# Kernel tuning notes

Measured on AMD Instinct MI355X. Metric: run time of the kernel, lower is better.

## Reference

```python
import jax, jax.numpy as jnp
import numpy as np

N, E, H, F, T = 50000, 800000, 64, 74, 4
STEPS = 4


def setup_inputs() -> dict:
    key = jax.random.key(0)
    ks = jax.random.split(key, 16)
    s = 0.05
    return {
        "x": jax.random.normal(ks[0], (N, F), jnp.float32),
        "etype": jax.random.randint(ks[1], (E,), 0, T, jnp.int32),
        "src": jax.random.randint(ks[2], (E,), 0, N, jnp.int32),
        "dst": jax.random.randint(ks[3], (E,), 0, N, jnp.int32),
        "W_in": jax.random.normal(ks[4], (F, H), jnp.float32) * s,
        "b_in": jax.random.normal(ks[5], (H,), jnp.float32) * s,
        "edge_W": jax.random.normal(ks[6], (T, H, H), jnp.float32) * s,
        "edge_b": jax.random.normal(ks[7], (T, 1), jnp.float32) * s,
        "gru_Wih": jax.random.normal(ks[8], (H, 3 * H), jnp.float32) * s,
        "gru_Whh": jax.random.normal(ks[9], (H, 3 * H), jnp.float32) * s,
        "gru_bih": jax.random.normal(ks[10], (3 * H,), jnp.float32) * s,
        "gru_bhh": jax.random.normal(ks[11], (3 * H,), jnp.float32) * s,
        "mlp_W1": jax.random.normal(ks[12], (2 * H, H), jnp.float32) * s,
        "mlp_b1": jax.random.normal(ks[13], (H,), jnp.float32) * s,
        "mlp_W2": jax.random.normal(ks[14], (H, H), jnp.float32) * s,
        "mlp_b2": jax.random.normal(ks[15], (H,), jnp.float32) * s,
    }


def _gru_cell(x, h, Wih, Whh, bih, bhh):
    gi = x @ Wih + bih  # [N, 3H]
    gh = h @ Whh + bhh
    ir, iz, inn = jnp.split(gi, 3, axis=-1)
    hr, hz, hn = jnp.split(gh, 3, axis=-1)
    r = jax.nn.sigmoid(ir + hr)
    z = jax.nn.sigmoid(iz + hz)
    n = jnp.tanh(inn + r * hn)
    return (1.0 - z) * n + z * h


def reference(x, etype, src, dst, W_in, b_in, edge_W, edge_b,
              gru_Wih, gru_Whh, gru_bih, gru_bhh,
              mlp_W1, mlp_b1, mlp_W2, mlp_b2):
    h_init = x @ W_in + b_in  # [N, H]
    h = h_init
    for _ in range(STEPS):
        # per-node transform under every edge type: [N, T, H]
        nt = jnp.einsum('ni,tio->nto', h, edge_W)
        # gather per-edge message from src node + per-type bias, ReLU
        msg = jax.nn.relu(nt[src, etype] + edge_b[etype])  # [E, H]
        agg = jax.ops.segment_sum(msg, dst, num_segments=N)  # [N, H]
        h = _gru_cell(agg, h, gru_Wih, gru_Whh, gru_bih, gru_bhh)
    cat = jnp.concatenate([h_init, h], axis=-1)  # [N, 2H]
    out = jnp.tanh(jax.nn.relu(cat @ mlp_W1 + mlp_b1) @ mlp_W2 + mlp_b2)
    return out
```

## Files before the change

kernel.cpp:

```cpp
#include <hip/hip_runtime.h>
#include <hip/hip_bf16.h>

#define N_NODES 50000
#define M2      50048
#define N_EDGES 800000
#define H 64
#define F 74
#define T 4
#define STEPS 4
#define NTILES16 (M2/16)
#define PAD_REC  (M2*4)
#define SCAN_NB  196

using short8 = __attribute__((ext_vector_type(8))) short;
using f32x4  = __attribute__((ext_vector_type(4))) float;
typedef unsigned short ushort_t;

#define MFMA(a,b,c) __builtin_amdgcn_mfma_f32_16x16x32_bf16(a,b,c,0,0,0)

static __device__ inline float b2f(ushort_t u) {
    union { unsigned int i; float f; } c; c.i = ((unsigned int)u) << 16; return c.f;
}
static __device__ inline ushort_t f2b(float v) {
    union { __hip_bfloat16 b; ushort_t u; } c; c.b = __float2bfloat16(v); return c.u;
}
static __device__ inline void split_store(ushort_t* hi, ushort_t* lo, size_t ix, float v) {
    ushort_t h = f2b(v);
    hi[ix] = h;
    lo[ix] = f2b(v - b2f(h));
}
static __device__ inline float sigm(float x) { return 1.f / (1.f + __expf(-x)); }
static __device__ inline float tanh_f(float x) {
    float e2 = __expf(2.f * x); return 1.f - 2.f / (e2 + 1.f);
}

template<int KW8>
static __device__ inline void stage_tile(const ushort_t* __restrict__ g, ushort_t* l,
                                         int rows, int tid, int nthr) {
    const int chunks = rows * KW8;
    for (int i = tid; i < chunks; i += nthr) {
        int row = i / KW8, kg = i - row * KW8;
        short8 v = *(const short8*)(g + (size_t)row * (KW8 * 8) + kg * 8);
        int b = (row * (KW8 * 16) + kg * 16) ^ ((row & 7) << 4);
        *(short8*)((char*)l + b) = v;
    }
}
template<int KW8>
static __device__ inline short8 rdfrag(const ushort_t* l, int row, int kg) {
    int b = (row * (KW8 * 16) + kg * 16) ^ ((row & 7) << 4);
    return *(const short8*)((const char*)l + b);
}
static __device__ inline short8 afrag(const ushort_t* base, int LD, int row, int kg) {
    return *(const short8*)(base + (size_t)row * LD + kg * 8);
}

__global__ __launch_bounds__(256) void prep_w_kernel(
    const float* __restrict__ W_in, const float* __restrict__ eW,
    const float* __restrict__ Wih, const float* __restrict__ Whh,
    const float* __restrict__ W1, const float* __restrict__ W2,
    const float* __restrict__ x,
    ushort_t* __restrict__ BtWin_hi, ushort_t* __restrict__ BtWin_lo,
    ushort_t* __restrict__ BtE_hi,
    ushort_t* __restrict__ BtgHi, ushort_t* __restrict__ BtgLo,
    ushort_t* __restrict__ BtW1_hi, ushort_t* __restrict__ BtW1_lo,
    ushort_t* __restrict__ BtW2_hi, ushort_t* __restrict__ BtW2_lo,
    int* __restrict__ deg, ushort_t* __restrict__ ntr_pad,
    ushort_t* __restrict__ x_hi, ushort_t* __restrict__ x_lo)
{
    int idx = blockIdx.x * 256 + threadIdx.x;
    if (idx < 6144) {
        int col = idx / 96, k = idx - col * 96;
        float v = (k < F) ? W_in[(size_t)k * 64 + col] : 0.f;
        split_store(BtWin_hi, BtWin_lo, idx, v);
    } else if (idx < 22528) {
        int i = idx - 6144;
        int c = i >> 6, k = i & 63;
        float v = eW[(c >> 6) * 4096 + k * 64 + (c & 63)];
        BtE_hi[i] = f2b(v);
    } else if (idx < 47104) {
        int i = idx - 22528;
        int hh = i / 12288;
        int r2 = i - hh * 12288;
        int rr = r2 >> 7, k = r2 & 127;
        int gg = rr >> 5, cc = rr & 31;
        int col = gg * 64 + hh * 32 + cc;
        float v = (k < 64) ? Wih[(size_t)k * 192 + col]
                           : Whh[(size_t)(k - 64) * 192 + col];
        BtgHi[i] = f2b(v);
    } else if (idx < 55296) {
        int i = idx - 47104;
        int hh = i >> 12;
        int r2 = i & 4095;
        int cc = r2 >> 7, k = r2 & 127;
        int col = 128 + hh * 32 + cc;
        float v = (k < 64) ? Wih[(size_t)k * 192 + col]
                           : Whh[(size_t)(k - 64) * 192 + col];
        ushort_t h = f2b(v);
        BtgLo[i] = f2b(v - b2f(h));
    } else if (idx < 63488) {
        int i = idx - 55296;
        int col = i >> 7, k = i & 127;
        float v = W1[(size_t)k * 64 + col];
        split_store(BtW1_hi, BtW1_lo, i, v);
    } else if (idx < 67584) {
        int i = idx - 63488;
        int col = i >> 6, k = i & 63;
        float v = W2[(size_t)k * 64 + col];
        split_store(BtW2_hi, BtW2_lo, i, v);
    } else if (idx < 117584) {
        deg[idx - 67584] = 0;
    } else if (idx < 117648) {
        ntr_pad[idx - 117584] = 0;
    } else {
        int i = idx - 117648;
        if (i < M2 * 96) {
            int row = i / 96, c = i - row * 96;
            float v = (row < N_NODES && c < F) ? x[(size_t)row * F + c] : 0.f;
            split_store(x_hi, x_lo, i, v);
        }
    }
}

__global__ __launch_bounds__(256) void degrank_kernel(
    const int* __restrict__ dst, int* __restrict__ deg, int* __restrict__ rank)
{
    int e = blockIdx.x * 256 + threadIdx.x;
    if (e < N_EDGES) rank[e] = atomicAdd(&deg[dst[e]], 1);
}

__global__ __launch_bounds__(256) void scan_p1(
    const int* __restrict__ deg, int* __restrict__ bsum)
{
    __shared__ int ws4[4];
    const int tid = threadIdx.x, lane = tid & 63, w = tid >> 6;
    int idx = blockIdx.x * 256 + tid;
    int v = (idx < N_NODES) ? deg[idx] : 0;
#pragma unroll
    for (int off = 32; off >= 1; off >>= 1) v += __shfl_down(v, off, 64);
    if (lane == 0) ws4[w] = v;
    __syncthreads();
    if (tid == 0) bsum[blockIdx.x] = ws4[0] + ws4[1] + ws4[2] + ws4[3];
}

__global__ __launch_bounds__(256) void scan_p2(
    const int* __restrict__ bsum, int* __restrict__ boff, int* __restrict__ rowp)
{
    __shared__ int ws4[4];
    const int tid = threadIdx.x, lane = tid & 63, w = tid >> 6;
    int v = (tid < SCAN_NB) ? bsum[tid] : 0;
    int x = v;
#pragma unroll
    for (int off = 1; off < 64; off <<= 1) {
        int u = __shfl_up(x, off, 64);
        if (lane >= off) x += u;
    }
    if (lane == 63) ws4[w] = x;
    __syncthreads();
    int a0 = ws4[0], a1 = ws4[1], a2 = ws4[2];
    int add = (w > 0 ? a0 : 0) + (w > 1 ? a1 : 0) + (w > 2 ? a2 : 0);
    if (tid < SCAN_NB) boff[tid] = add + x - v;
    if (tid == 255) rowp[N_NODES] = add + x;
}

__global__ __launch_bounds__(256) void scan_p3(
    const int* __restrict__ deg, const int* __restrict__ boff,
    int* __restrict__ rowp)
{
    __shared__ int ws4[4];
    const int tid = threadIdx.x, lane = tid & 63, w = tid >> 6;
    int idx = blockIdx.x * 256 + tid;
    int v = (idx < N_NODES) ? deg[idx] : 0;
    int x = v;
#pragma unroll
    for (int off = 1; off < 64; off <<= 1) {
        int u = __shfl_up(x, off, 64);
        if (lane >= off) x += u;
    }
    if (lane == 63) ws4[w] = x;
    __syncthreads();
    int a0 = ws4[0], a1 = ws4[1], a2 = ws4[2];
    int add = boff[blockIdx.x]
            + (w > 0 ? a0 : 0) + (w > 1 ? a1 : 0) + (w > 2 ? a2 : 0);
    if (idx < N_NODES) rowp[idx] = add + x - v;
}

__global__ __launch_bounds__(256) void fill2_kernel(
    const int* __restrict__ src, const int* __restrict__ etype,
    const int* __restrict__ dst, const int* __restrict__ rowp,
    const int* __restrict__ rank, int* __restrict__ ss)
{
    int e = blockIdx.x * 256 + threadIdx.x;
    if (e < N_EDGES)
        ss[rowp[dst[e]] + rank[e]] = src[e] * 4 + etype[e];
}

__global__ __launch_bounds__(256) void init_gemm(
    const ushort_t* __restrict__ xhi, const ushort_t* __restrict__ xlo,
    const ushort_t* __restrict__ Bh, const ushort_t* __restrict__ Bl,
    const float* __restrict__ b_in,
    ushort_t* __restrict__ h_hi, ushort_t* __restrict__ h_lo,
    ushort_t* __restrict__ hin_hi, ushort_t* __restrict__ hin_lo)
{
    __shared__ ushort_t lds[12288];
    ushort_t* LBh = lds;
    ushort_t* LBl = lds + 6144;
    const int tid = threadIdx.x, lane = tid & 63, wid = tid >> 6;
    const int lr = lane & 15, g = lane >> 4;
    stage_tile<12>(Bh, LBh, 64, tid, 256);
    stage_tile<12>(Bl, LBl, 64, tid, 256);
    __syncthreads();
    for (int wt = blockIdx.x * 4 + wid; wt < NTILES16; wt += gridDim.x * 4) {
        const ushort_t* pAh = xhi + (size_t)wt * 16 * 96;
        const ushort_t* pAl = xlo + (size_t)wt * 16 * 96;
        f32x4 acc[4];
        f32x4 zz = {0.f, 0.f, 0.f, 0.f};
#pragma unroll
        for (int f = 0; f < 4; ++f) acc[f] = zz;
#pragma unroll
        for (int ks = 0; ks < 3; ++ks) {
            int kg = ks * 4 + g;
            short8 ah = afrag(pAh, 96, lr, kg);
            short8 al = afrag(pAl, 96, lr, kg);
#pragma unroll
            for (int f = 0; f < 4; ++f) {
                short8 bh = rdfrag<12>(LBh, f * 16 + lr, kg);
                short8 bl = rdfrag<12>(LBl, f * 16 + lr, kg);
                acc[f] = MFMA(ah, bh, acc[f]);
                acc[f] = MFMA(ah, bl, acc[f]);
                acc[f] = MFMA(al, bh, acc[f]);
            }
        }
#pragma unroll
        for (int f = 0; f < 4; ++f) {
            int o = lr + f * 16;
            float b = b_in[o];
#pragma unroll
            for (int q = 0; q < 4; ++q) {
                int m = wt * 16 + g * 4 + q;
                if (m < N_NODES) {
                    float v = acc[f][q] + b;
                    split_store(h_hi, h_lo, (size_t)m * 64 + o, v);
                    split_store(hin_hi, hin_lo, (size_t)m * 64 + o, v);
                }
            }
        }
    }
}

__global__ __launch_bounds__(512, 2) void nt_gemm(
    const ushort_t* __restrict__ hhi,
    const ushort_t* __restrict__ Bh,
    const float* __restrict__ edge_b, ushort_t* __restrict__ ntr)
{
    __shared__ ushort_t lds[16384];
    const int tid = threadIdx.x, lane = tid & 63, wid = tid >> 6;
    const int lr = lane & 15, g = lane >> 4;
    stage_tile<8>(Bh, lds, 256, tid, 512);
    __syncthreads();
    for (int wt = blockIdx.x * 8 + wid; wt < NTILES16; wt += gridDim.x * 8) {
        const ushort_t* pA = hhi + (size_t)wt * 16 * 64;
        f32x4 acc[16];
        f32x4 zz = {0.f, 0.f, 0.f, 0.f};
#pragma unroll
        for (int f = 0; f < 16; ++f) acc[f] = zz;
#pragma unroll
        for (int ks = 0; ks < 2; ++ks) {
            int kg = ks * 4 + g;
            short8 ah = afrag(pA, 64, lr, kg);
#pragma unroll
            for (int f = 0; f < 16; ++f) {
                short8 bh = rdfrag<8>(lds, f * 16 + lr, kg);
                acc[f] = MFMA(ah, bh, acc[f]);
            }
        }
#pragma unroll
        for (int f = 0; f < 16; ++f) {
            int colg = lr + f * 16;
            float b = edge_b[colg >> 6];
#pragma unroll
            for (int q = 0; q < 4; ++q) {
                int m = wt * 16 + g * 4 + q;
                if (m < N_NODES) {
                    float v = fmaxf(acc[f][q] + b, 0.f);
                    ntr[(size_t)m * 256 + colg] = f2b(v);
                }
            }
        }
    }
}

__global__ __launch_bounds__(512, 2) void aggru_gemm(
    const ushort_t* __restrict__ ntr, const int* __restrict__ rowp,
    const int* __restrict__ ss,
    const ushort_t* __restrict__ Xhi, const ushort_t* __restrict__ Xlo,
    const ushort_t* __restrict__ BtgHi,
    const ushort_t* __restrict__ BtgLo,
    const float* __restrict__ bih, const float* __restrict__ bhh,
    ushort_t* __restrict__ Yhi, ushort_t* __restrict__ Ylo)
{
    __shared__ ushort_t ldsB[24576];
    __shared__ ushort_t aggh[4096];
    __shared__ ushort_t aggl[4096];
    const int tid = threadIdx.x, lane = tid & 63, wid = tid >> 6;
    const int lr = lane & 15, g = lane >> 4;
    stage_tile<16>(BtgHi, ldsB, 192, tid, 512);

    const int base = blockIdx.x * 64;
#pragma unroll 1
    for (int j = 0; j < 8; ++j) {
        int r = wid * 8 + j;
        int d = base + r;
        float acc = 0.f;
        if (d < N_NODES) {
            const int beg = rowp[d];
            const int end = rowp[d + 1];
            for (int p = beg; p < end; p += 16) {
                float v[16];
#pragma unroll
                for (int i = 0; i < 16; ++i) {
                    bool inb = (p + i) < end;
                    int rec = ss[inb ? (p + i) : beg];
                    rec = inb ? rec : PAD_REC;
                    v[i] = b2f(ntr[(size_t)rec * 64 + lane]);
                }
                float s0 = (v[0] + v[1]) + (v[2] + v[3]);
                float s1 = (v[4] + v[5]) + (v[6] + v[7]);
                float s2 = (v[8] + v[9]) + (v[10] + v[11]);
                float s3 = (v[12] + v[13]) + (v[14] + v[15]);
                acc += (s0 + s1) + (s2 + s3);
            }
        }
        int byt = (r * 128 + lane * 2) ^ ((r & 7) << 4);
        ushort_t hv = f2b(acc);
        *(ushort_t*)((char*)aggh + byt) = hv;
        *(ushort_t*)((char*)aggl + byt) = f2b(acc - b2f(hv));
    }
    __syncthreads();

    const int rt = wid & 3, hh = wid >> 2;
    const int ooff = hh * 32;
    const int bb = hh * 96;
    const int wt = blockIdx.x * 4 + rt;
    const ushort_t* pXh = Xhi + (size_t)wt * 16 * 64;
    const ushort_t* pXl = Xlo + (size_t)wt * 16 * 64;
    const ushort_t* pBln = BtgLo + (size_t)hh * 32 * 128;
    f32x4 aR[2], aZ[2], aIN[2], aHN[2];
    f32x4 zz = {0.f, 0.f, 0.f, 0.f};
#pragma unroll
    for (int f = 0; f < 2; ++f) { aR[f] = zz; aZ[f] = zz; aIN[f] = zz; aHN[f] = zz; }
#pragma unroll
    for (int ks = 0; ks < 4; ++ks) {
        int kg = ks * 4 + g;
        short8 ah, al;
        if (ks < 2) {
            int arow = rt * 16 + lr;
            ah = rdfrag<8>(aggh, arow, kg);
            al = rdfrag<8>(aggl, arow, kg);
        } else {
            ah = afrag(pXh, 64, lr, kg - 8);
            al = afrag(pXl, 64, lr, kg - 8);
        }
#pragma unroll
        for (int f = 0; f < 2; ++f) {
            short8 bhr = rdfrag<16>(ldsB, bb + f * 16 + lr, kg);
            aR[f] = MFMA(ah, bhr, aR[f]);
            aR[f] = MFMA(al, bhr, aR[f]);
            short8 bhz = rdfrag<16>(ldsB, bb + 32 + f * 16 + lr, kg);
            aZ[f] = MFMA(ah, bhz, aZ[f]);
            aZ[f] = MFMA(al, bhz, aZ[f]);
            short8 bhn = rdfrag<16>(ldsB, bb + 64 + f * 16 + lr, kg);
            short8 bln = afrag(pBln, 128, f * 16 + lr, kg);
            if (ks < 2) {
                aIN[f] = MFMA(ah, bhn, aIN[f]);
                aIN[f] = MFMA(al, bhn, aIN[f]);
                aIN[f] = MFMA(ah, bln, aIN[f]);
            } else {
                aHN[f] = MFMA(ah, bhn, aHN[f]);
                aHN[f] = MFMA(al, bhn, aHN[f]);
                aHN[f] = MFMA(ah, bln, aHN[f]);
            }
        }
    }
#pragma unroll
    for (int f = 0; f < 2; ++f) {
        int o = ooff + f * 16 + lr;
        float br = bih[o] + bhh[o];
        float bz = bih[64 + o] + bhh[64 + o];
        float bi_n = bih[128 + o];
        float bh_n = bhh[128 + o];
#pragma unroll
        for (int q = 0; q < 4; ++q) {
            int m = wt * 16 + g * 4 + q;
            if (m < N_NODES) {
                float r = sigm(aR[f][q] + br);
                float z = sigm(aZ[f][q] + bz);
                float inn = aIN[f][q] + bi_n;
                float hn = aHN[f][q] + bh_n;
                float nn = tanh_f(inn + r * hn);
                size_t hix = (size_t)m * 64 + o;
                float hp = b2f(Xhi[hix]) + b2f(Xlo[hix]);
                float hv = (1.f - z) * nn + z * hp;
                split_store(Yhi, Ylo, hix, hv);
            }
        }
    }
}

__global__ __launch_bounds__(256) void mlp_fused(
    const ushort_t* __restrict__ hin_hi, const ushort_t* __restrict__ hin_lo,
    const ushort_t* __restrict__ hhi, const ushort_t* __restrict__ hlo,
    const ushort_t* __restrict__ B1h, const ushort_t* __restrict__ B1l,
    const float* __restrict__ b1,
    const ushort_t* __restrict__ B2h, const ushort_t* __restrict__ B2l,
    const float* __restrict__ b2, float* __restrict__ out)
{
    __shared__ ushort_t l1h[8192];
    __shared__ ushort_t l1l[8192];
    __shared__ ushort_t l2h[4096];
    __shared__ ushort_t l2l[4096];
    __shared__ ushort_t th[4][1024];
    __shared__ ushort_t tl[4][1024];
    const int tid = threadIdx.x, lane = tid & 63, wid = tid >> 6;
    const int lr = lane & 15, g = lane >> 4;
    stage_tile<16>(B1h, l1h, 64, tid, 256);
    stage_tile<16>(B1l, l1l, 64, tid, 256);
    stage_tile<8>(B2h, l2h, 64, tid, 256);
    stage_tile<8>(B2l, l2l, 64, tid, 256);
    __syncthreads();
    char* myh = (char*)th[wid];
    char* myl = (char*)tl[wid];
    for (int wt = blockIdx.x * 4 + wid; wt < NTILES16; wt += gridDim.x * 4) {
        const ushort_t* pAh0 = hin_hi + (size_t)wt * 16 * 64;
        const ushort_t* pAl0 = hin_lo + (size_t)wt * 16 * 64;
        const ushort_t* pAh1 = hhi + (size_t)wt * 16 * 64;
        const ushort_t* pAl1 = hlo + (size_t)wt * 16 * 64;
        f32x4 acc[4];
        f32x4 zz = {0.f, 0.f, 0.f, 0.f};
#pragma unroll
        for (int f = 0; f < 4; ++f) acc[f] = zz;
#pragma unroll
        for (int ks = 0; ks < 4; ++ks) {
            int kg = ks * 4 + g;
            short8 ah, al;
            if (ks < 2) {
                ah = afrag(pAh0, 64, lr, kg);
                al = afrag(pAl0, 64, lr, kg);
            } else {
                ah = afrag(pAh1, 64, lr, kg - 8);
                al = afrag(pAl1, 64, lr, kg - 8);
            }
#pragma unroll
            for (int f = 0; f < 4; ++f) {
                short8 bh = rdfrag<16>(l1h, f * 16 + lr, kg);
                short8 bl = rdfrag<16>(l1l, f * 16 + lr, kg);
                acc[f] = MFMA(ah, bh, acc[f]);
                acc[f] = MFMA(ah, bl, acc[f]);
                acc[f] = MFMA(al, bh, acc[f]);
            }
        }
#pragma unroll
        for (int f = 0; f < 4; ++f) {
            int col = f * 16 + lr;
            float b = b1[col];
#pragma unroll
            for (int q = 0; q < 4; ++q) {
                int row = g * 4 + q;
                float v = fmaxf(acc[f][q] + b, 0.f);
                int byt = (row * 128 + col * 2) ^ ((row & 7) << 4);
                ushort_t hv = f2b(v);
                *(ushort_t*)(myh + byt) = hv;
                *(ushort_t*)(myl + byt) = f2b(v - b2f(hv));
            }
        }
        f32x4 acc2[4];
#pragma unroll
        for (int f = 0; f < 4; ++f) acc2[f] = zz;
#pragma unroll
        for (int ks = 0; ks < 2; ++ks) {
            int kg = ks * 4 + g;
            int byt = (lr * 128 + kg * 16) ^ ((lr & 7) << 4);
            short8 ah = *(const short8*)(myh + byt);
            short8 al = *(const short8*)(myl + byt);
#pragma unroll
            for (int f = 0; f < 4; ++f) {
                short8 bh = rdfrag<8>(l2h, f * 16 + lr, kg);
                short8 bl = rdfrag<8>(l2l, f * 16 + lr, kg);
                acc2[f] = MFMA(ah, bh, acc2[f]);
                acc2[f] = MFMA(ah, bl, acc2[f]);
                acc2[f] = MFMA(al, bh, acc2[f]);
            }
        }
#pragma unroll
        for (int f = 0; f < 4; ++f) {
            int o = lr + f * 16;
            float b = b2[o];
#pragma unroll
            for (int q = 0; q < 4; ++q) {
                int m = wt * 16 + g * 4 + q;
                if (m < N_NODES)
                    out[(size_t)m * 64 + o] = tanh_f(acc2[f][q] + b);
            }
        }
    }
}

extern "C" void kernel_launch(void* const* d_in, const int* in_sizes, int n_in,
                              void* d_out, int out_size, void* d_ws, size_t ws_size,
                              hipStream_t stream)
{
    const float* x      = (const float*)d_in[0];
    const int*   etype  = (const int*)  d_in[1];
    const int*   src    = (const int*)  d_in[2];
    const int*   dst    = (const int*)  d_in[3];
    const float* W_in   = (const float*)d_in[4];
    const float* b_in   = (const float*)d_in[5];
    const float* edge_W = (const float*)d_in[6];
    const float* edge_b = (const float*)d_in[7];
    const float* gWih   = (const float*)d_in[8];
    const float* gWhh   = (const float*)d_in[9];
    const float* gbih   = (const float*)d_in[10];
    const float* gbhh   = (const float*)d_in[11];
    const float* W1     = (const float*)d_in[12];
    const float* b1     = (const float*)d_in[13];
    const float* W2     = (const float*)d_in[14];
    const float* b2     = (const float*)d_in[15];
    float* out = (float*)d_out;

    char* ws = (char*)d_ws;
    ushort_t* ntr    = (ushort_t*)(ws);
    ushort_t* x_hi   = (ushort_t*)(ws);
    ushort_t* x_lo   = (ushort_t*)(ws + 9609216);
    int*      rank   = (int*)     (ws + 19660800);
    ushort_t* hA_hi  = (ushort_t*)(ws + 25625088);
    ushort_t* hA_lo  = (ushort_t*)(ws + 32031232);
    ushort_t* hB_hi  = (ushort_t*)(ws + 38437376);
    ushort_t* hB_lo  = (ushort_t*)(ws + 44843520);
    ushort_t* hin_hi = (ushort_t*)(ws + 51249664);
    ushort_t* hin_lo = (ushort_t*)(ws + 57655808);
    char* wbase = ws + 64061952;
    ushort_t* BtWin_hi = (ushort_t*)(wbase);
    ushort_t* BtWin_lo = (ushort_t*)(wbase + 12288);
    ushort_t* BtE_hi   = (ushort_t*)(wbase + 24576);
    ushort_t* BtgHi    = (ushort_t*)(wbase + 57344);
    ushort_t* BtgLo    = (ushort_t*)(wbase + 106496);
    ushort_t* BtW1_hi  = (ushort_t*)(wbase + 122880);
    ushort_t* BtW1_lo  = (ushort_t*)(wbase + 139264);
    ushort_t* BtW2_hi  = (ushort_t*)(wbase + 155648);
    ushort_t* BtW2_lo  = (ushort_t*)(wbase + 163840);
    char* cbase = ws + 64233984;
    int* deg    = (int*)(cbase);
    int* rowp   = (int*)(cbase + 200192);
    int* ss     = (int*)(cbase + 400640);
    int* bsum   = (int*)(cbase + 3600640);
    int* boff   = (int*)(cbase + 3601664);

    const int edge_tblocks = (N_EDGES + 255) / 256;
    const int GB  = 782;
    const int GB8 = 512;
    ushort_t* ntr_pad = ntr + (size_t)M2 * 256;

    const int PREP_TOTAL = 117648 + M2 * 96;
    prep_w_kernel<<<(PREP_TOTAL + 255) / 256, 256, 0, stream>>>(
        W_in, edge_W, gWih, gWhh, W1, W2, x,
        BtWin_hi, BtWin_lo, BtE_hi, BtgHi, BtgLo,
        BtW1_hi, BtW1_lo, BtW2_hi, BtW2_lo,
        deg, ntr_pad, x_hi, x_lo);

    degrank_kernel<<<edge_tblocks, 256, 0, stream>>>(dst, deg, rank);
    scan_p1<<<SCAN_NB, 256, 0, stream>>>(deg, bsum);
    scan_p2<<<1, 256, 0, stream>>>(bsum, boff, rowp);
    scan_p3<<<SCAN_NB, 256, 0, stream>>>(deg, boff, rowp);
    fill2_kernel<<<edge_tblocks, 256, 0, stream>>>(src, etype, dst, rowp, rank, ss);

    init_gemm<<<GB, 256, 0, stream>>>(x_hi, x_lo, BtWin_hi, BtWin_lo, b_in,
                                      hA_hi, hA_lo, hin_hi, hin_lo);

    ushort_t *Xhi = hA_hi, *Xlo = hA_lo, *Yhi = hB_hi, *Ylo = hB_lo;
    for (int s = 0; s < STEPS; ++s) {
        nt_gemm<<<GB8, 512, 0, stream>>>(Xhi, BtE_hi, edge_b, ntr);
        aggru_gemm<<<GB, 512, 0, stream>>>(ntr, rowp, ss, Xhi, Xlo,
                                           BtgHi, BtgLo, gbih, gbhh, Yhi, Ylo);
        ushort_t* t;
        t = Xhi; Xhi = Yhi; Yhi = t;
        t = Xlo; Xlo = Ylo; Ylo = t;
    }

    mlp_fused<<<GB, 256, 0, stream>>>(hin_hi, hin_lo, Xhi, Xlo,
                                      BtW1_hi, BtW1_lo, b1,
                                      BtW2_hi, BtW2_lo, b2, out);
}
```

Baseline: 402.3 us.

## Split fused aggregate+GRU kernel into separate gather kernel and persistent GRU GEMM

Moves the segment-sum gather out of the fused aggru kernel into its own kernel, with one wave per destination node and small blocks for higher occupancy. The aggregate is written to global memory as hi/lo bf16. A persistent GRU GEMM then loops over tiles and keeps all gate weights in LDS, including the n-gate low-precision part that was previously read from global memory. This is meant to stop the irregular gather from serialising behind the GEMM's LDS use and low occupancy. In exchange it adds an extra global write and read of the aggregate and one more kernel launch per step.

Measured after the change: 365.2 us (median of 2 runs). -9.2%, faster.

```diff
diff --git a/kernel.cpp b/kernel.cpp
--- a/kernel.cpp
+++ b/kernel.cpp
@@ -61,7 +61,7 @@
     const float* __restrict__ x,
     ushort_t* __restrict__ BtWin_hi, ushort_t* __restrict__ BtWin_lo,
     ushort_t* __restrict__ BtE_hi,
-    ushort_t* __restrict__ BtgHi, ushort_t* __restrict__ BtgLo,
+    ushort_t* __restrict__ Btg_all,
     ushort_t* __restrict__ BtW1_hi, ushort_t* __restrict__ BtW1_lo,
     ushort_t* __restrict__ BtW2_hi, ushort_t* __restrict__ BtW2_lo,
     int* __restrict__ deg, ushort_t* __restrict__ ntr_pad,
@@ -77,26 +77,18 @@
         int c = i >> 6, k = i & 63;
         float v = eW[(c >> 6) * 4096 + k * 64 + (c & 63)];
         BtE_hi[i] = f2b(v);
-    } else if (idx < 47104) {
+    } else if (idx < 55296) {
         int i = idx - 22528;
-        int hh = i / 12288;
-        int r2 = i - hh * 12288;
+        int hh = i >> 14;
+        int r2 = i & 16383;
         int rr = r2 >> 7, k = r2 & 127;
-        int gg = rr >> 5, cc = rr & 31;
-        int col = gg * 64 + hh * 32 + cc;
-        float v = (k < 64) ? Wih[(size_t)k * 192 + col]
-                           : Whh[(size_t)(k - 64) * 192 + col];
-        BtgHi[i] = f2b(v);
-    } else if (idx < 55296) {
-        int i = idx - 47104;
-        int hh = i >> 12;
-        int r2 = i & 4095;
-        int cc = r2 >> 7, k = r2 & 127;
-        int col = 128 + hh * 32 + cc;
+        int g = rr >> 5, cc = rr & 31;
+        int gate = (g == 3) ? 2 : g;
+        int col = gate * 64 + hh * 32 + cc;
         float v = (k < 64) ? Wih[(size_t)k * 192 + col]
                            : Whh[(size_t)(k - 64) * 192 + col];
         ushort_t h = f2b(v);
-        BtgLo[i] = f2b(v - b2f(h));
+        Btg_all[i] = (g == 3) ? f2b(v - b2f(h)) : h;
     } else if (idx < 63488) {
         int i = idx - 55296;
         int col = i >> 7, k = i & 127;
@@ -289,118 +281,114 @@
     }
 }
 
-__global__ __launch_bounds__(512, 2) void aggru_gemm(
-    const ushort_t* __restrict__ ntr, const int* __restrict__ rowp,
-    const int* __restrict__ ss,
+__global__ __launch_bounds__(256, 4) void agg_kernel(
+    const ushort_t* __restrict__ ntr, const int* __restrict__ row_ptr,
+    const int* __restrict__ ss, ushort_t* __restrict__ agg_hi,
+    ushort_t* __restrict__ agg_lo)
+{
+    const int lane = threadIdx.x & 63;
+    const int w = __builtin_amdgcn_readfirstlane((int)(threadIdx.x >> 6));
+    const int d = blockIdx.x * 4 + w;
+    if (d >= N_NODES) return;
+    const int beg = row_ptr[d];
+    const int end = row_ptr[d + 1];
+    float acc = 0.f;
+    for (int p = beg; p < end; p += 16) {
+        float v[16];
+#pragma unroll
+        for (int i = 0; i < 16; ++i) {
+            bool inb = (p + i) < end;
+            int rec = ss[inb ? (p + i) : beg];
+            rec = inb ? rec : PAD_REC;
+            v[i] = b2f(ntr[(size_t)rec * 64 + lane]);
+        }
+        float s0 = (v[0] + v[1]) + (v[2] + v[3]);
+        float s1 = (v[4] + v[5]) + (v[6] + v[7]);
+        float s2 = (v[8] + v[9]) + (v[10] + v[11]);
+        float s3 = (v[12] + v[13]) + (v[14] + v[15]);
+        acc += (s0 + s1) + (s2 + s3);
+    }
+    split_store(agg_hi, agg_lo, (size_t)d * 64 + lane, acc);
+}
+
+__global__ __launch_bounds__(512, 2) void gru3_gemm(
+    const ushort_t* __restrict__ agg_hi, const ushort_t* __restrict__ agg_lo,
     const ushort_t* __restrict__ Xhi, const ushort_t* __restrict__ Xlo,
-    const ushort_t* __restrict__ BtgHi,
-    const ushort_t* __restrict__ BtgLo,
+    const ushort_t* __restrict__ Btg,
     const float* __restrict__ bih, const float* __restrict__ bhh,
     ushort_t* __restrict__ Yhi, ushort_t* __restrict__ Ylo)
 {
-    __shared__ ushort_t ldsB[24576];
-    __shared__ ushort_t aggh[4096];
-    __shared__ ushort_t aggl[4096];
+    __shared__ ushort_t lds[32768];
     const int tid = threadIdx.x, lane = tid & 63, wid = tid >> 6;
     const int lr = lane & 15, g = lane >> 4;
-    stage_tile<16>(BtgHi, ldsB, 192, tid, 512);
-
-    const int base = blockIdx.x * 64;
-#pragma unroll 1
-    for (int j = 0; j < 8; ++j) {
-        int r = wid * 8 + j;
-        int d = base + r;
-        float acc = 0.f;
-        if (d < N_NODES) {
-            const int beg = rowp[d];
-            const int end = rowp[d + 1];
-            for (int p = beg; p < end; p += 16) {
-                float v[16];
-#pragma unroll
-                for (int i = 0; i < 16; ++i) {
-                    bool inb = (p + i) < end;
-                    int rec = ss[inb ? (p + i) : beg];
-                    rec = inb ? rec : PAD_REC;
-                    v[i] = b2f(ntr[(size_t)rec * 64 + lane]);
+    stage_tile<16>(Btg, lds, 256, tid, 512);
+    __syncthreads();
+    const int hh = wid >> 2;
+    const int ooff = hh * 32;
+    const int bb = hh * 128;
+    for (int wt0 = blockIdx.x * 4; wt0 < NTILES16; wt0 += gridDim.x * 4) {
+        const int wt = wt0 + (wid & 3);
+        const ushort_t* pGh = agg_hi + (size_t)wt * 16 * 64;
+        const ushort_t* pGl = agg_lo + (size_t)wt * 16 * 64;
+        const ushort_t* pXh = Xhi + (size_t)wt * 16 * 64;
+        const ushort_t* pXl = Xlo + (size_t)wt * 16 * 64;
+        f32x4 aR[2], aZ[2], aIN[2], aHN[2];
+        f32x4 zz = {0.f, 0.f, 0.f, 0.f};
+#pragma unroll
+        for (int f = 0; f < 2; ++f) { aR[f] = zz; aZ[f] = zz; aIN[f] = zz; aHN[f] = zz; }
+#pragma unroll
+        for (int ks = 0; ks < 4; ++ks) {
+            int kg = ks * 4 + g;
+            short8 ah, al;
+            if (ks < 2) {
+                ah = afrag(pGh, 64, lr, kg);
+                al = afrag(pGl, 64, lr, kg);
+            } else {
+                ah = afrag(pXh, 64, lr, kg - 8);
+                al = afrag(pXl, 64, lr, kg - 8);
+            }
+#pragma unroll
+            for (int f = 0; f < 2; ++f) {
+                short8 bhr = rdfrag<16>(lds, bb + f * 16 + lr, kg);
+                aR[f] = MFMA(ah, bhr, aR[f]);
+                aR[f] = MFMA(al, bhr, aR[f]);
+                short8 bhz = rdfrag<16>(lds, bb + 32 + f * 16 + lr, kg);
+                aZ[f] = MFMA(ah, bhz, aZ[f]);
+                aZ[f] = MFMA(al, bhz, aZ[f]);
+                short8 bhn = rdfrag<16>(lds, bb + 64 + f * 16 + lr, kg);
+                short8 bln = rdfrag<16>(lds, bb + 96 + f * 16 + lr, kg);
+                if (ks < 2) {
+                    aIN[f] = MFMA(ah, bhn, aIN[f]);
+                    aIN[f] = MFMA(al, bhn, aIN[f]);
+                    aIN[f] = MFMA(ah, bln, aIN[f]);
+                } else {
+                    aHN[f] = MFMA(ah, bhn, aHN[f]);
+                    aHN[f] = MFMA(al, bhn, aHN[f]);
+                    aHN[f] = MFMA(ah, bln, aHN[f]);
                 }
-                float s0 = (v[0] + v[1]) + (v[2] + v[3]);
-                float s1 = (v[4] + v[5]) + (v[6] + v[7]);
-                float s2 = (v[8] + v[9]) + (v[10] + v[11]);
-                float s3 = (v[12] + v[13]) + (v[14] + v[15]);
-                acc += (s0 + s1) + (s2 + s3);
-            }
-        }
-        int byt = (r * 128 + lane * 2) ^ ((r & 7) << 4);
-        ushort_t hv = f2b(acc);
-        *(ushort_t*)((char*)aggh + byt) = hv;
-        *(ushort_t*)((char*)aggl + byt) = f2b(acc - b2f(hv));
-    }
-    __syncthreads();
-
-    const int rt = wid & 3, hh = wid >> 2;
-    const int ooff = hh * 32;
-    const int bb = hh * 96;
-    const int wt = blockIdx.x * 4 + rt;
-    const ushort_t* pXh = Xhi + (size_t)wt * 16 * 64;
-    const ushort_t* pXl = Xlo + (size_t)wt * 16 * 64;
-    const ushort_t* pBln = BtgLo + (size_t)hh * 32 * 128;
-    f32x4 aR[2], aZ[2], aIN[2], aHN[2];
-    f32x4 zz = {0.f, 0.f, 0.f, 0.f};
-#pragma unroll
-    for (int f = 0; f < 2; ++f) { aR[f] = zz; aZ[f] = zz; aIN[f] = zz; aHN[f] = zz; }
-#pragma unroll
-    for (int ks = 0; ks < 4; ++ks) {
-        int kg = ks * 4 + g;
-        short8 ah, al;
-        if (ks < 2) {
-            int arow = rt * 16 + lr;
-            ah = rdfrag<8>(aggh, arow, kg);
-            al = rdfrag<8>(aggl, arow, kg);
-        } else {
-            ah = afrag(pXh, 64, lr, kg - 8);
-            al = afrag(pXl, 64, lr, kg - 8);
+            }
         }
 #pragma unroll
         for (int f = 0; f < 2; ++f) {
-            short8 bhr = rdfrag<16>(ldsB, bb + f * 16 + lr, kg);
-            aR[f] = MFMA(ah, bhr, aR[f]);
-            aR[f] = MFMA(al, bhr, aR[f]);
-            short8 bhz = rdfrag<16>(ldsB, bb + 32 + f * 16 + lr, kg);
-            aZ[f] = MFMA(ah, bhz, aZ[f]);
-            aZ[f] = MFMA(al, bhz, aZ[f]);
-            short8 bhn = rdfrag<16>(ldsB, bb + 64 + f * 16 + lr, kg);
-            short8 bln = afrag(pBln, 128, f * 16 + lr, kg);
-            if (ks < 2) {
-                aIN[f] = MFMA(ah, bhn, aIN[f]);
-                aIN[f] = MFMA(al, bhn, aIN[f]);
-                aIN[f] = MFMA(ah, bln, aIN[f]);
-            } else {
-                aHN[f] = MFMA(ah, bhn, aHN[f]);
-                aHN[f] = MFMA(al, bhn, aHN[f]);
-                aHN[f] = MFMA(ah, bln, aHN[f]);
-            }
-        }
-    }
-#pragma unroll
-    for (int f = 0; f < 2; ++f) {
-        int o = ooff + f * 16 + lr;
-        float br = bih[o] + bhh[o];
-        float bz = bih[64 + o] + bhh[64 + o];
-        float bi_n = bih[128 + o];
-        float bh_n = bhh[128 + o];
-#pragma unroll
-        for (int q = 0; q < 4; ++q) {
-            int m = wt * 16 + g * 4 + q;
-            if (m < N_NODES) {
-                float r = sigm(aR[f][q] + br);
-                float z = sigm(aZ[f][q] + bz);
-                float inn = aIN[f][q] + bi_n;
-                float hn = aHN[f][q] + bh_n;
-                float nn = tanh_f(inn + r * hn);
-                size_t hix = (size_t)m * 64 + o;
-                float hp = b2f(Xhi[hix]) + b2f(Xlo[hix]);
-                float hv = (1.f - z) * nn + z * hp;
-                split_store(Yhi, Ylo, hix, hv);
+            int o = ooff + f * 16 + lr;
+            float br = bih[o] + bhh[o];
+            float bz = bih[64 + o] + bhh[64 + o];
+            float bi_n = bih[128 + o];
+            float bh_n = bhh[128 + o];
+#pragma unroll
+            for (int q = 0; q < 4; ++q) {
+                int m = wt * 16 + g * 4 + q;
+                if (m < N_NODES) {
+                    float r = sigm(aR[f][q] + br);
+                    float z = sigm(aZ[f][q] + bz);
+                    float inn = aIN[f][q] + bi_n;
+                    float hn = aHN[f][q] + bh_n;
+                    float nn = tanh_f(inn + r * hn);
+                    size_t hix = (size_t)m * 64 + o;
+                    float hp = b2f(Xhi[hix]) + b2f(Xlo[hix]);
+                    float hv = (1.f - z) * nn + z * hp;
+                    split_store(Yhi, Ylo, hix, hv);
+                }
             }
         }
     }
@@ -537,17 +525,18 @@
     ushort_t* hB_lo  = (ushort_t*)(ws + 44843520);
     ushort_t* hin_hi = (ushort_t*)(ws + 51249664);
     ushort_t* hin_lo = (ushort_t*)(ws + 57655808);
-    char* wbase = ws + 64061952;
+    ushort_t* agg_hi = (ushort_t*)(ws + 64061952);
+    ushort_t* agg_lo = (ushort_t*)(ws + 70468096);
+    char* wbase = ws + 76874240;
     ushort_t* BtWin_hi = (ushort_t*)(wbase);
     ushort_t* BtWin_lo = (ushort_t*)(wbase + 12288);
     ushort_t* BtE_hi   = (ushort_t*)(wbase + 24576);
-    ushort_t* BtgHi    = (ushort_t*)(wbase + 57344);
-    ushort_t* BtgLo    = (ushort_t*)(wbase + 106496);
+    ushort_t* Btg_all  = (ushort_t*)(wbase + 57344);
     ushort_t* BtW1_hi  = (ushort_t*)(wbase + 122880);
     ushort_t* BtW1_lo  = (ushort_t*)(wbase + 139264);
     ushort_t* BtW2_hi  = (ushort_t*)(wbase + 155648);
     ushort_t* BtW2_lo  = (ushort_t*)(wbase + 163840);
-    char* cbase = ws + 64233984;
+    char* cbase = ws + 77046272;
     int* deg    = (int*)(cbase);
     int* rowp   = (int*)(cbase + 200192);
     int* ss     = (int*)(cbase + 400640);
@@ -555,14 +544,16 @@
     int* boff   = (int*)(cbase + 3601664);
 
     const int edge_tblocks = (N_EDGES + 255) / 256;
+    const int agg_blocks = (N_NODES + 3) / 4;
     const int GB  = 782;
     const int GB8 = 512;
+    const int GBF = 512;
     ushort_t* ntr_pad = ntr + (size_t)M2 * 256;
 
     const int PREP_TOTAL = 117648 + M2 * 96;
     prep_w_kernel<<<(PREP_TOTAL + 255) / 256, 256, 0, stream>>>(
         W_in, edge_W, gWih, gWhh, W1, W2, x,
-        BtWin_hi, BtWin_lo, BtE_hi, BtgHi, BtgLo,
+        BtWin_hi, BtWin_lo, BtE_hi, Btg_all,
         BtW1_hi, BtW1_lo, BtW2_hi, BtW2_lo,
         deg, ntr_pad, x_hi, x_lo);
 
@@ -578,8 +569,9 @@
     ushort_t *Xhi = hA_hi, *Xlo = hA_lo, *Yhi = hB_hi, *Ylo = hB_lo;
     for (int s = 0; s < STEPS; ++s) {
         nt_gemm<<<GB8, 512, 0, stream>>>(Xhi, BtE_hi, edge_b, ntr);
-        aggru_gemm<<<GB, 512, 0, stream>>>(ntr, rowp, ss, Xhi, Xlo,
-                                           BtgHi, BtgLo, gbih, gbhh, Yhi, Ylo);
+        agg_kernel<<<agg_blocks, 256, 0, stream>>>(ntr, rowp, ss, agg_hi, agg_lo);
+        gru3_gemm<<<GBF, 512, 0, stream>>>(agg_hi, agg_lo, Xhi, Xlo,
+                                           Btg_all, gbih, gbhh, Yhi, Ylo);
         ushort_t* t;
         t = Xhi; Xhi = Yhi; Yhi = t;
         t = Xlo; Xlo = Ylo; Ylo = t;
```
